# Optimization experiments

Hardware: AMD Instinct MI355X
Metric: run time of the kernel (lower is better)

## Reference

```python
import jax, jax.numpy as jnp
import numpy as np

N_NODES = 100000
N_EDGES = 3200000
N_GRAPHS = 128


def setup_inputs() -> dict:
    key = jax.random.key(0)
    ks = jax.random.split(key, 16)
    x = jax.random.normal(ks[0], (N_NODES, 47), dtype=jnp.float32)
    edge_index = jax.random.randint(ks[1], (2, N_EDGES), 0, N_NODES, dtype=jnp.int32)
    batch = jnp.sort(jax.random.randint(ks[2], (N_NODES,), 0, N_GRAPHS, dtype=jnp.int32))

    def w(k, shape):
        fan_in = shape[0]
        return jax.random.normal(k, shape, dtype=jnp.float32) * (1.0 / np.sqrt(fan_in))

    return {
        "x": x, "edge_index": edge_index, "batch": batch,
        "W1": w(ks[3], (47, 64)), "b1": jnp.zeros((64,), jnp.float32),
        "W2": w(ks[4], (64, 32)), "b2": jnp.zeros((32,), jnp.float32),
        "A1": w(ks[5], (32, 32)), "c1": jnp.zeros((32,), jnp.float32),
        "A2": w(ks[6], (32, 16)), "c2": jnp.zeros((16,), jnp.float32),
        "A3": w(ks[7], (16, 8)),  "c3": jnp.zeros((8,), jnp.float32),
        "A4": w(ks[8], (8, 1)),   "c4": jnp.zeros((1,), jnp.float32),
    }


def _gcn_conv(x, W, b, src, dst):
    # PyG GCNConv: h = XW, then D^-1/2 (A+I) D^-1/2 aggregation, then + bias.
    h = x @ W  # [N, out]
    ones = jnp.ones(dst.shape[0], dtype=h.dtype)
    deg = jax.ops.segment_sum(ones, dst, num_segments=N_NODES)  # incl. self loops
    dinv = jnp.where(deg > 0, jax.lax.rsqrt(deg), 0.0)
    norm = dinv[src] * dinv[dst]  # [E_total]
    msg = h[src] * norm[:, None]  # gather + normalize
    out = jax.ops.segment_sum(msg, dst, num_segments=N_NODES)  # scatter-add
    return out + b


def reference(x, edge_index, batch, W1, b1, W2, b2, A1, c1, A2, c2, A3, c3, A4, c4):
    loops = jnp.arange(N_NODES, dtype=edge_index.dtype)
    src = jnp.concatenate([edge_index[0], loops])
    dst = jnp.concatenate([edge_index[1], loops])
    h = jax.nn.relu(_gcn_conv(x, W1, b1, src, dst))
    h = jax.nn.relu(_gcn_conv(h, W2, b2, src, dst))
    # dropout is identity in eval mode
    g = jax.ops.segment_sum(h, batch, num_segments=N_GRAPHS)  # global_add_pool [G,32]
    g = jax.nn.relu(g @ A1 + c1)
    g = jax.nn.relu(g @ A2 + c2)
    g = jax.nn.relu(g @ A3 + c3)
    return g @ A4 + c4  # [G, 1]
```

## Files before the change

### kernel.cpp

```cpp
#include <hip/hip_runtime.h>

#define N_NODES 100000
#define N_EDGES 3200000
#define N_GRAPHS 128

#define RSHIFT 8
#define NPR 256
#define R_RANGES ((N_NODES + NPR - 1) / NPR)
#define CAP 9472
#define C_CHUNKS 512
#define EPC (N_EDGES / C_CHUNKS)
#define SRC_BITS 17

#define XPB 64
#define AXW 48

__device__ inline unsigned short f2bf(float f) {
    unsigned u = __float_as_uint(f);
    unsigned r = u + 0x7FFFu + ((u >> 16) & 1u);
    return (unsigned short)(r >> 16);
}
__device__ inline float bflo(unsigned u) { return __uint_as_float(u << 16); }
__device__ inline float bfhi(unsigned u) { return __uint_as_float(u & 0xFFFF0000u); }


__global__ __launch_bounds__(256) void padcvt_kernel(const float* __restrict__ x,
                                                     unsigned short* __restrict__ xpb,
                                                     int* __restrict__ range_next) {
    if (blockIdx.x < 2) {
        int i = blockIdx.x * 256 + threadIdx.x;
        if (i < R_RANGES) range_next[i] = i * CAP;
    }
    int idx = blockIdx.x * 256 + threadIdx.x;
    if (idx >= N_NODES * XPB) return;
    int n = idx >> 6;
    int c = idx & 63;
    float v = (c < 47) ? x[n * 47 + c] : 0.f;
    xpb[idx] = f2bf(v);
}


__global__ __launch_bounds__(256) void partition_kernel(const int* __restrict__ src,
                                                        const int* __restrict__ dst,
                                                        int* __restrict__ range_next,
                                                        int* __restrict__ bucket) {
    __shared__ int cntL[R_RANGES];
    __shared__ int baseL[R_RANGES];
    const int t = threadIdx.x, b = blockIdx.x;
    const int e0 = b * EPC, e1 = e0 + EPC;
    for (int i = t; i < R_RANGES; i += 256) cntL[i] = 0;
    __syncthreads();
    for (int e = e0 + t; e < e1; e += 256) atomicAdd(&cntL[dst[e] >> RSHIFT], 1);
    __syncthreads();
    for (int i = t; i < R_RANGES; i += 256) {
        int c = cntL[i];
        baseL[i] = (c > 0) ? atomicAdd(&range_next[i], c) : 0;
        cntL[i] = 0;
    }
    __syncthreads();
    for (int e = e0 + t; e < e1; e += 256) {
        int d = dst[e];
        int s = src[e];
        int r = d >> RSHIFT;
        int p = baseL[r] + atomicAdd(&cntL[r], 1);
        if (p < (r + 1) * CAP)
            bucket[p] = ((d & (NPR - 1)) << SRC_BITS) | s;
    }
}


__global__ __launch_bounds__(256) void build_kernel(const int* __restrict__ bucket,
                                                    const int* __restrict__ range_next,
                                                    int* __restrict__ row_ptr,
                                                    int* __restrict__ row_cnt,
                                                    float* __restrict__ dinv,
                                                    int* __restrict__ csr_src) {
    __shared__ int sE[CAP];
    __shared__ int degs[NPR];
    __shared__ int part[256];
    const int t = threadIdx.x, r = blockIdx.x;
    const int base_node = r * NPR;
    const int seg0 = r * CAP;
    int m = range_next[r] - seg0;
    if (m > CAP) m = CAP;
    for (int i = t; i < m; i += 256) sE[i] = bucket[seg0 + i];
    degs[t] = 0;
    __syncthreads();
    for (int i = t; i < m; i += 256) atomicAdd(&degs[sE[i] >> SRC_BITS], 1);
    __syncthreads();
    int d = degs[t];
    part[t] = d;
    __syncthreads();
    for (int dd = 1; dd < 256; dd <<= 1) {
        int tv = (t >= dd) ? part[t - dd] : 0;
        __syncthreads();
        part[t] += tv;
        __syncthreads();
    }
    int ex = part[t] - d;
    int node = base_node + t;
    if (node < N_NODES) {
        row_ptr[node] = seg0 + ex;
        row_cnt[node] = d;
        dinv[node] = rsqrtf((float)(d + 1));
    }
    degs[t] = ex;
    __syncthreads();
    for (int i = t; i < m; i += 256) {
        int p = sE[i];
        int pos = atomicAdd(&degs[p >> SRC_BITS], 1);
        csr_src[seg0 + pos] = p & ((1 << SRC_BITS) - 1);
    }
}


__global__ __launch_bounds__(256) void wprep_kernel(const int* __restrict__ csr_src,
                                                    const int* __restrict__ range_next,
                                                    const float* __restrict__ dinv,
                                                    float* __restrict__ csr_w) {
    const int t = threadIdx.x, r = blockIdx.x;
    const int seg0 = r * CAP;
    int m = range_next[r] - seg0;
    if (m > CAP) m = CAP;
    for (int i = t; i < m; i += 256) {
        csr_w[seg0 + i] = dinv[csr_src[seg0 + i]];
    }
}


__global__ __launch_bounds__(256) void aggX_kernel(const unsigned short* __restrict__ xpb,
                                                   const float* __restrict__ dinv,
                                                   const int* __restrict__ row_ptr,
                                                   const int* __restrict__ row_cnt,
                                                   const int* __restrict__ csr_src,
                                                   const float* __restrict__ csr_w,
                                                   unsigned short* __restrict__ aggxb) {
    const int tid = threadIdx.x;
    const int n = blockIdx.x * 4 + (tid >> 6);
    if (n >= N_NODES) return;
    const int l = tid & 63;
    const int eo = l >> 3;
    const int cg = l & 7;
    const float dn = dinv[n];

    float acc[8] = {0.f, 0.f, 0.f, 0.f, 0.f, 0.f, 0.f, 0.f};
    if (eo == 0) {
        uint4 q = *(const uint4*)(xpb + (size_t)n * XPB + cg * 8);
        float w = dn * dn;
        acc[0] = bflo(q.x) * w; acc[1] = bfhi(q.x) * w;
        acc[2] = bflo(q.y) * w; acc[3] = bfhi(q.y) * w;
        acc[4] = bflo(q.z) * w; acc[5] = bfhi(q.z) * w;
        acc[6] = bflo(q.w) * w; acc[7] = bfhi(q.w) * w;
    }
    const int st = row_ptr[n];
    const int cnt = row_cnt[n];
    int k = eo;
    for (; k + 8 < cnt; k += 16) {
        int s0 = csr_src[st + k];
        int s1 = csr_src[st + k + 8];
        float w0 = csr_w[st + k] * dn;
        float w1 = csr_w[st + k + 8] * dn;
        uint4 q0 = *(const uint4*)(xpb + (size_t)s0 * XPB + cg * 8);
        uint4 q1 = *(const uint4*)(xpb + (size_t)s1 * XPB + cg * 8);
        acc[0] = fmaf(bflo(q0.x), w0, acc[0]); acc[1] = fmaf(bfhi(q0.x), w0, acc[1]);
        acc[2] = fmaf(bflo(q0.y), w0, acc[2]); acc[3] = fmaf(bfhi(q0.y), w0, acc[3]);
        acc[4] = fmaf(bflo(q0.z), w0, acc[4]); acc[5] = fmaf(bfhi(q0.z), w0, acc[5]);
        acc[6] = fmaf(bflo(q0.w), w0, acc[6]); acc[7] = fmaf(bfhi(q0.w), w0, acc[7]);
        acc[0] = fmaf(bflo(q1.x), w1, acc[0]); acc[1] = fmaf(bfhi(q1.x), w1, acc[1]);
        acc[2] = fmaf(bflo(q1.y), w1, acc[2]); acc[3] = fmaf(bfhi(q1.y), w1, acc[3]);
        acc[4] = fmaf(bflo(q1.z), w1, acc[4]); acc[5] = fmaf(bfhi(q1.z), w1, acc[5]);
        acc[6] = fmaf(bflo(q1.w), w1, acc[6]); acc[7] = fmaf(bfhi(q1.w), w1, acc[7]);
    }
    if (k < cnt) {
        int s0 = csr_src[st + k];
        float w0 = csr_w[st + k] * dn;
        uint4 q0 = *(const uint4*)(xpb + (size_t)s0 * XPB + cg * 8);
        acc[0] = fmaf(bflo(q0.x), w0, acc[0]); acc[1] = fmaf(bfhi(q0.x), w0, acc[1]);
        acc[2] = fmaf(bflo(q0.y), w0, acc[2]); acc[3] = fmaf(bfhi(q0.y), w0, acc[3]);
        acc[4] = fmaf(bflo(q0.z), w0, acc[4]); acc[5] = fmaf(bfhi(q0.z), w0, acc[5]);
        acc[6] = fmaf(bflo(q0.w), w0, acc[6]); acc[7] = fmaf(bfhi(q0.w), w0, acc[7]);
    }
#pragma unroll
    for (int off = 8; off <= 32; off <<= 1) {
#pragma unroll
        for (int j = 0; j < 8; ++j) acc[j] += __shfl_xor(acc[j], off);
    }
    if (eo == 0 && cg < 6) {
        uint4 o;
        o.x = ((unsigned)f2bf(acc[1]) << 16) | f2bf(acc[0]);
        o.y = ((unsigned)f2bf(acc[3]) << 16) | f2bf(acc[2]);
        o.z = ((unsigned)f2bf(acc[5]) << 16) | f2bf(acc[4]);
        o.w = ((unsigned)f2bf(acc[7]) << 16) | f2bf(acc[6]);
        *(uint4*)(aggxb + (size_t)n * AXW + cg * 8) = o;
    }
}


#define GB_NODES 100

__global__ __launch_bounds__(256) void fusedgemm_kernel(const unsigned short* __restrict__ aggxb,
                                                        const float* __restrict__ W1,
                                                        const float* __restrict__ b1,
                                                        const float* __restrict__ W2,
                                                        unsigned short* __restrict__ zb) {
    __shared__ float W1s[AXW * 64];
    __shared__ float W2s[64 * 32];
    __shared__ float b1s[64];
    __shared__ float rows[4][AXW];
    __shared__ float ts[4][64];
    const int t = threadIdx.x;
    for (int i = t; i < 47 * 64; i += 256) W1s[i] = W1[i];
    for (int i = t; i < 64; i += 256) { W1s[47 * 64 + i] = 0.f; b1s[i] = b1[i]; }
    for (int i = t; i < 64 * 32; i += 256) W2s[i] = W2[i];
    __syncthreads();

    const int base = blockIdx.x * GB_NODES;
    for (int pass = 0; pass < GB_NODES / 4; ++pass) {
        const int nb = base + pass * 4;
        if (t < 4 * AXW) {
            rows[t / AXW][t % AXW] = bflo(aggxb[(size_t)nb * AXW + t]);
        }
        __syncthreads();
        {
            const int nn = t >> 6, c = t & 63;
            float s = b1s[c];
#pragma unroll
            for (int k = 0; k < AXW; ++k) s = fmaf(rows[nn][k], W1s[k * 64 + c], s);
            ts[nn][c] = fmaxf(s, 0.f);
        }
        __syncthreads();
        if (t < 128) {
            const int nn = t >> 5, c = t & 31;
            float s = 0.f;
#pragma unroll
            for (int k = 0; k < 64; ++k) s = fmaf(ts[nn][k], W2s[k * 32 + c], s);
            zb[(size_t)(nb + nn) * 32 + c] = f2bf(s);
        }
        __syncthreads();
    }
}


__global__ __launch_bounds__(256) void aggregate32_kernel(const unsigned short* __restrict__ zb,
                                                          const float* __restrict__ dinv,
                                                          const int* __restrict__ row_ptr,
                                                          const int* __restrict__ row_cnt,
                                                          const int* __restrict__ csr_src,
                                                          const float* __restrict__ csr_w,
                                                          const float* __restrict__ bias,
                                                          float* __restrict__ out) {
    const int tid = threadIdx.x;
    const int n = blockIdx.x * 4 + (tid >> 6);
    if (n >= N_NODES) return;
    const int l = tid & 63;
    const int eo = l >> 2;
    const int cg = l & 3;
    const float dn = dinv[n];

    float acc[8] = {0.f, 0.f, 0.f, 0.f, 0.f, 0.f, 0.f, 0.f};
    if (eo == 0) {
        uint4 q = *(const uint4*)(zb + (size_t)n * 32 + cg * 8);
        float w = dn * dn;
        acc[0] = bflo(q.x) * w; acc[1] = bfhi(q.x) * w;
        acc[2] = bflo(q.y) * w; acc[3] = bfhi(q.y) * w;
        acc[4] = bflo(q.z) * w; acc[5] = bfhi(q.z) * w;
        acc[6] = bflo(q.w) * w; acc[7] = bfhi(q.w) * w;
    }
    const int st = row_ptr[n];
    const int cnt = row_cnt[n];
    int k = eo;
    for (; k + 16 < cnt; k += 32) {
        int s0 = csr_src[st + k];
        int s1 = csr_src[st + k + 16];
        float w0 = csr_w[st + k] * dn;
        float w1 = csr_w[st + k + 16] * dn;
        uint4 q0 = *(const uint4*)(zb + (size_t)s0 * 32 + cg * 8);
        uint4 q1 = *(const uint4*)(zb + (size_t)s1 * 32 + cg * 8);
        acc[0] = fmaf(bflo(q0.x), w0, acc[0]); acc[1] = fmaf(bfhi(q0.x), w0, acc[1]);
        acc[2] = fmaf(bflo(q0.y), w0, acc[2]); acc[3] = fmaf(bfhi(q0.y), w0, acc[3]);
        acc[4] = fmaf(bflo(q0.z), w0, acc[4]); acc[5] = fmaf(bfhi(q0.z), w0, acc[5]);
        acc[6] = fmaf(bflo(q0.w), w0, acc[6]); acc[7] = fmaf(bfhi(q0.w), w0, acc[7]);
        acc[0] = fmaf(bflo(q1.x), w1, acc[0]); acc[1] = fmaf(bfhi(q1.x), w1, acc[1]);
        acc[2] = fmaf(bflo(q1.y), w1, acc[2]); acc[3] = fmaf(bfhi(q1.y), w1, acc[3]);
        acc[4] = fmaf(bflo(q1.z), w1, acc[4]); acc[5] = fmaf(bfhi(q1.z), w1, acc[5]);
        acc[6] = fmaf(bflo(q1.w), w1, acc[6]); acc[7] = fmaf(bfhi(q1.w), w1, acc[7]);
    }
    if (k < cnt) {
        int s0 = csr_src[st + k];
        float w0 = csr_w[st + k] * dn;
        uint4 q0 = *(const uint4*)(zb + (size_t)s0 * 32 + cg * 8);
        acc[0] = fmaf(bflo(q0.x), w0, acc[0]); acc[1] = fmaf(bfhi(q0.x), w0, acc[1]);
        acc[2] = fmaf(bflo(q0.y), w0, acc[2]); acc[3] = fmaf(bfhi(q0.y), w0, acc[3]);
        acc[4] = fmaf(bflo(q0.z), w0, acc[4]); acc[5] = fmaf(bfhi(q0.z), w0, acc[5]);
        acc[6] = fmaf(bflo(q0.w), w0, acc[6]); acc[7] = fmaf(bfhi(q0.w), w0, acc[7]);
    }
#pragma unroll
    for (int off = 4; off <= 32; off <<= 1) {
#pragma unroll
        for (int j = 0; j < 8; ++j) acc[j] += __shfl_xor(acc[j], off);
    }
    if (eo == 0) {
        const float* bp = bias + cg * 8;
        float4 a, b;
        a.x = fmaxf(acc[0] + bp[0], 0.f);
        a.y = fmaxf(acc[1] + bp[1], 0.f);
        a.z = fmaxf(acc[2] + bp[2], 0.f);
        a.w = fmaxf(acc[3] + bp[3], 0.f);
        b.x = fmaxf(acc[4] + bp[4], 0.f);
        b.y = fmaxf(acc[5] + bp[5], 0.f);
        b.z = fmaxf(acc[6] + bp[6], 0.f);
        b.w = fmaxf(acc[7] + bp[7], 0.f);
        *(float4*)(out + (size_t)n * 32 + cg * 8) = a;
        *(float4*)(out + (size_t)n * 32 + cg * 8 + 4) = b;
    }
}


#define POOL_NPB 256

__global__ __launch_bounds__(256) void pool_kernel(const int* __restrict__ batch,
                                                   const float* __restrict__ h,
                                                   float* __restrict__ g) {
    const int t = threadIdx.x;
    const int c = t & 31;
    const int r = t >> 5;
    int i0 = blockIdx.x * POOL_NPB;
    int i1 = i0 + POOL_NPB;
    if (i1 > N_NODES) i1 = N_NODES;
    int cur_g = -1;
    float acc = 0.f;
    for (int i = i0 + r; i < i1; i += 8) {
        int gi = batch[i];
        float v = h[(size_t)i * 32 + c];
        if (gi != cur_g) {
            if (cur_g >= 0) atomicAdd(&g[cur_g * 32 + c], acc);
            acc = 0.f;
            cur_g = gi;
        }
        acc += v;
    }
    if (cur_g >= 0) atomicAdd(&g[cur_g * 32 + c], acc);
}


__global__ __launch_bounds__(128) void mlp_kernel(const float* __restrict__ g,
                                                  const float* __restrict__ A1, const float* __restrict__ c1,
                                                  const float* __restrict__ A2, const float* __restrict__ c2,
                                                  const float* __restrict__ A3, const float* __restrict__ c3,
                                                  const float* __restrict__ A4, const float* __restrict__ c4,
                                                  float* __restrict__ out) {
    int t = threadIdx.x;
    float v[32];
#pragma unroll
    for (int k = 0; k < 32; ++k) v[k] = g[t * 32 + k];
    float u[32];
#pragma unroll
    for (int c = 0; c < 32; ++c) {
        float s = c1[c];
#pragma unroll
        for (int k = 0; k < 32; ++k) s = fmaf(v[k], A1[k * 32 + c], s);
        u[c] = fmaxf(s, 0.f);
    }
    float w[16];
#pragma unroll
    for (int c = 0; c < 16; ++c) {
        float s = c2[c];
#pragma unroll
        for (int k = 0; k < 32; ++k) s = fmaf(u[k], A2[k * 16 + c], s);
        w[c] = fmaxf(s, 0.f);
    }
    float z[8];
#pragma unroll
    for (int c = 0; c < 8; ++c) {
        float s = c3[c];
#pragma unroll
        for (int k = 0; k < 16; ++k) s = fmaf(w[k], A3[k * 8 + c], s);
        z[c] = fmaxf(s, 0.f);
    }
    float s = c4[0];
#pragma unroll
    for (int k = 0; k < 8; ++k) s = fmaf(z[k], A4[k], s);
    out[t] = s;
}


extern "C" void kernel_launch(void* const* d_in, const int* in_sizes, int n_in,
                              void* d_out, int out_size, void* d_ws, size_t ws_size,
                              hipStream_t stream) {
    const float* x    = (const float*)d_in[0];
    const int*   ei   = (const int*)d_in[1];
    const int*   srcE = ei;
    const int*   dstE = ei + N_EDGES;
    const int*   batch = (const int*)d_in[2];
    const float* W1 = (const float*)d_in[3];  const float* b1 = (const float*)d_in[4];
    const float* W2 = (const float*)d_in[5];  const float* b2 = (const float*)d_in[6];
    const float* A1 = (const float*)d_in[7];  const float* c1 = (const float*)d_in[8];
    const float* A2 = (const float*)d_in[9];  const float* c2 = (const float*)d_in[10];
    const float* A3 = (const float*)d_in[11]; const float* c3 = (const float*)d_in[12];
    const float* A4 = (const float*)d_in[13]; const float* c4 = (const float*)d_in[14];
    float* out = (float*)d_out;

    char* ws = (char*)d_ws;
    size_t off_b = 0;
    auto take = [&](size_t bytes) -> char* {
        char* p = ws + off_b;
        off_b = (off_b + bytes + 255) & ~(size_t)255;
        return p;
    };
    int*            row_ptr    = (int*)take((size_t)N_NODES * 4);
    int*            row_cnt    = (int*)take((size_t)N_NODES * 4);
    float*          dinv       = (float*)take((size_t)N_NODES * 4);
    int*            range_next = (int*)take((size_t)R_RANGES * 4);
    int*            csr_src    = (int*)take((size_t)R_RANGES * CAP * 4);
    float*          csr_w      = (float*)take((size_t)R_RANGES * CAP * 4);
    char*           bz_raw     = take((size_t)R_RANGES * CAP * 4);
    int*            bucket     = (int*)bz_raw;
    unsigned short* zb         = (unsigned short*)bz_raw;
    unsigned short* xpb        = (unsigned short*)take((size_t)N_NODES * XPB * 2);
    char*           aa_raw     = take((size_t)N_NODES * 32 * 4);
    unsigned short* aggxb      = (unsigned short*)aa_raw;
    float*          agg        = (float*)aa_raw;
    float*          g          = (float*)take((size_t)N_GRAPHS * 32 * 4);
    (void)ws_size; (void)in_sizes; (void)n_in; (void)out_size;

    padcvt_kernel<<<(N_NODES * XPB + 255) / 256, 256, 0, stream>>>(x, xpb, range_next);

    partition_kernel<<<C_CHUNKS, 256, 0, stream>>>(srcE, dstE, range_next, bucket);
    build_kernel<<<R_RANGES, 256, 0, stream>>>(bucket, range_next, row_ptr, row_cnt, dinv, csr_src);
    wprep_kernel<<<R_RANGES, 256, 0, stream>>>(csr_src, range_next, dinv, csr_w);

    aggX_kernel<<<(N_NODES + 3) / 4, 256, 0, stream>>>(xpb, dinv, row_ptr, row_cnt, csr_src, csr_w, aggxb);
    fusedgemm_kernel<<<N_NODES / GB_NODES, 256, 0, stream>>>(aggxb, W1, b1, W2, zb);
    aggregate32_kernel<<<(N_NODES + 3) / 4, 256, 0, stream>>>(zb, dinv, row_ptr, row_cnt, csr_src, csr_w, b2, agg);

    hipMemsetAsync(g, 0, (size_t)N_GRAPHS * 32 * 4, stream);
    pool_kernel<<<(N_NODES + POOL_NPB - 1) / POOL_NPB, 256, 0, stream>>>(batch, agg, g);
    mlp_kernel<<<1, 128, 0, stream>>>(g, A1, c1, A2, c2, A3, c3, A4, c4, out);
}
```

Baseline: 390.3 us.

## Restructure fused GEMM as per-wavefront tiles without block syncs; double partition chunks

The fused two-layer GEMM kernel now gives each wavefront its own 16 nodes, processed 4 at a time. The weights are stored transposed and padded in shared memory so each lane reads float4 vectors, and each weight load is reused across 4 rows. This removes the block-wide __syncthreads between stages and cuts redundant LDS traffic. The partition kernel's chunk count is also doubled for more parallelism, at the cost of more atomic contention on range counters. Correctness within a wavefront relies on its lanes executing in lockstep when sharing the LDS rows and ts buffers, since no barrier separates them.

```diff
diff --git a/kernel.cpp b/kernel.cpp
--- a/kernel.cpp
+++ b/kernel.cpp
@@ -8,7 +8,7 @@
 #define NPR 256
 #define R_RANGES ((N_NODES + NPR - 1) / NPR)
 #define CAP 9472
-#define C_CHUNKS 512
+#define C_CHUNKS 1024
 #define EPC (N_EDGES / C_CHUNKS)
 #define SRC_BITS 17
 
@@ -196,47 +196,70 @@
 }
 
 
-#define GB_NODES 100
+#define FGW1 52
+#define FGW2 68
 
 __global__ __launch_bounds__(256) void fusedgemm_kernel(const unsigned short* __restrict__ aggxb,
                                                         const float* __restrict__ W1,
                                                         const float* __restrict__ b1,
                                                         const float* __restrict__ W2,
                                                         unsigned short* __restrict__ zb) {
-    __shared__ float W1s[AXW * 64];
-    __shared__ float W2s[64 * 32];
+    __shared__ float W1t[64 * FGW1];
+    __shared__ float W2t[32 * FGW2];
     __shared__ float b1s[64];
-    __shared__ float rows[4][AXW];
-    __shared__ float ts[4][64];
+    __shared__ float rows[4][4][48];
+    __shared__ float ts[4][4][64];
     const int t = threadIdx.x;
-    for (int i = t; i < 47 * 64; i += 256) W1s[i] = W1[i];
-    for (int i = t; i < 64; i += 256) { W1s[47 * 64 + i] = 0.f; b1s[i] = b1[i]; }
-    for (int i = t; i < 64 * 32; i += 256) W2s[i] = W2[i];
-    __syncthreads();
-
-    const int base = blockIdx.x * GB_NODES;
-    for (int pass = 0; pass < GB_NODES / 4; ++pass) {
-        const int nb = base + pass * 4;
-        if (t < 4 * AXW) {
-            rows[t / AXW][t % AXW] = bflo(aggxb[(size_t)nb * AXW + t]);
+    for (int i = t; i < 48 * 64; i += 256) { int k = i >> 6, c = i & 63; W1t[c * FGW1 + k] = W1[i]; }
+    for (int i = t; i < 64 * 32; i += 256) { int k = i >> 5, c = i & 31; W2t[c * FGW2 + k] = W2[i]; }
+    if (t < 64) b1s[t] = b1[t];
+    __syncthreads();
+
+    const int w = t >> 6, l = t & 63;
+    const int nb0 = blockIdx.x * 64 + w * 16;
+    const float* wc1 = &W1t[l * FGW1];
+    const int nn = l >> 5, c2 = l & 31;
+    const float* wc2 = &W2t[c2 * FGW2];
+
+    for (int p = 0; p < 4; ++p) {
+        const int n0 = nb0 + p * 4;
+        if (n0 >= N_NODES) break;
+        if (l < 48) {
+#pragma unroll
+            for (int j = 0; j < 4; ++j)
+                rows[w][j][l] = bflo(aggxb[(size_t)(n0 + j) * AXW + l]);
         }
-        __syncthreads();
         {
-            const int nn = t >> 6, c = t & 63;
-            float s = b1s[c];
-#pragma unroll
-            for (int k = 0; k < AXW; ++k) s = fmaf(rows[nn][k], W1s[k * 64 + c], s);
-            ts[nn][c] = fmaxf(s, 0.f);
+            float h0 = b1s[l], h1 = h0, h2 = h0, h3 = h0;
+#pragma unroll
+            for (int k4 = 0; k4 < 48; k4 += 4) {
+                float4 wv = *(const float4*)(wc1 + k4);
+                float4 r0 = *(const float4*)&rows[w][0][k4];
+                float4 r1 = *(const float4*)&rows[w][1][k4];
+                float4 r2 = *(const float4*)&rows[w][2][k4];
+                float4 r3 = *(const float4*)&rows[w][3][k4];
+                h0 = fmaf(r0.x, wv.x, h0); h0 = fmaf(r0.y, wv.y, h0); h0 = fmaf(r0.z, wv.z, h0); h0 = fmaf(r0.w, wv.w, h0);
+                h1 = fmaf(r1.x, wv.x, h1); h1 = fmaf(r1.y, wv.y, h1); h1 = fmaf(r1.z, wv.z, h1); h1 = fmaf(r1.w, wv.w, h1);
+                h2 = fmaf(r2.x, wv.x, h2); h2 = fmaf(r2.y, wv.y, h2); h2 = fmaf(r2.z, wv.z, h2); h2 = fmaf(r2.w, wv.w, h2);
+                h3 = fmaf(r3.x, wv.x, h3); h3 = fmaf(r3.y, wv.y, h3); h3 = fmaf(r3.z, wv.z, h3); h3 = fmaf(r3.w, wv.w, h3);
+            }
+            ts[w][0][l] = fmaxf(h0, 0.f);
+            ts[w][1][l] = fmaxf(h1, 0.f);
+            ts[w][2][l] = fmaxf(h2, 0.f);
+            ts[w][3][l] = fmaxf(h3, 0.f);
         }
-        __syncthreads();
-        if (t < 128) {
-            const int nn = t >> 5, c = t & 31;
-            float s = 0.f;
-#pragma unroll
-            for (int k = 0; k < 64; ++k) s = fmaf(ts[nn][k], W2s[k * 32 + c], s);
-            zb[(size_t)(nb + nn) * 32 + c] = f2bf(s);
+#pragma unroll
+        for (int sp = 0; sp < 2; ++sp) {
+            const float* tv = ts[w][sp * 2 + nn];
+            float z = 0.f;
+#pragma unroll
+            for (int k4 = 0; k4 < 64; k4 += 4) {
+                float4 a = *(const float4*)(tv + k4);
+                float4 wv = *(const float4*)(wc2 + k4);
+                z = fmaf(a.x, wv.x, z); z = fmaf(a.y, wv.y, z); z = fmaf(a.z, wv.z, z); z = fmaf(a.w, wv.w, z);
+            }
+            zb[(size_t)(n0 + sp * 2 + nn) * 32 + c2] = f2bf(z);
         }
-        __syncthreads();
     }
 }
 
@@ -430,7 +453,7 @@
     wprep_kernel<<<R_RANGES, 256, 0, stream>>>(csr_src, range_next, dinv, csr_w);
 
     aggX_kernel<<<(N_NODES + 3) / 4, 256, 0, stream>>>(xpb, dinv, row_ptr, row_cnt, csr_src, csr_w, aggxb);
-    fusedgemm_kernel<<<N_NODES / GB_NODES, 256, 0, stream>>>(aggxb, W1, b1, W2, zb);
+    fusedgemm_kernel<<<(N_NODES + 63) / 64, 256, 0, stream>>>(aggxb, W1, b1, W2, zb);
     aggregate32_kernel<<<(N_NODES + 3) / 4, 256, 0, stream>>>(zb, dinv, row_ptr, row_cnt, csr_src, csr_w, b2, agg);
 
     hipMemsetAsync(g, 0, (size_t)N_GRAPHS * 32 * 4, stream);
```

Result: slower. 398.6 us (+2.1%).
